# Kernel optimization log

Hardware: AMD Instinct MI355X
Metric: run time of the kernel (lower is better)

Reference implementation:

```python
import jax, jax.numpy as jnp
import numpy as np

B, N, D, H = 8, 1024, 512, 8
HD = D // H
SCALE = 1.0 / np.sqrt(HD).astype(np.float32)


def setup_inputs() -> dict:
    key = jax.random.key(0)
    ks = jax.random.split(key, 7)
    x = jax.random.normal(ks[0], (B, N, D), dtype=jnp.float32)
    U = jax.random.normal(ks[1], (N, N), dtype=jnp.float32)
    attn_mask = jax.random.uniform(ks[2], (B, 1, 1, N), dtype=jnp.float32)
    # learned params: qkv projection D->3D and output projection D->D (with bias)
    w_qkv = jax.random.normal(ks[3], (D, 3 * D), dtype=jnp.float32) / np.sqrt(D).astype(np.float32)
    b_qkv = jnp.zeros((3 * D,), dtype=jnp.float32)
    w_out = jax.random.normal(ks[4], (D, D), dtype=jnp.float32) / np.sqrt(D).astype(np.float32)
    b_out = jnp.zeros((D,), dtype=jnp.float32)
    return {"x": x, "U": U, "attn_mask": attn_mask,
            "w_qkv": w_qkv, "b_qkv": b_qkv, "w_out": w_out, "b_out": b_out}


def reference(x, U, attn_mask, w_qkv, b_qkv, w_out, b_out):
    # QKV projection (QuantIdentity layers are identity in math; key_value = x)
    qkv = x @ w_qkv + b_qkv                       # [B, N, 3D]
    q, k, v = jnp.split(qkv, 3, axis=-1)          # each [B, N, D]

    def split_heads(t):
        return t.reshape(B, N, H, HD).transpose(0, 2, 1, 3)  # [B, H, N, HD]

    qh, kh, vh = split_heads(q), split_heads(k), split_heads(v)
    scores = jnp.einsum('bhqd,bhkd->bhqk', qh, kh) * SCALE   # [B, H, N, N]
    scores = scores + U[None, None, :, :]                    # additive interaction bias
    scores = scores + attn_mask                              # [B,1,1,N] broadcast add
    attn = jax.nn.softmax(scores, axis=-1)
    ctx = jnp.einsum('bhqk,bhkd->bhqd', attn, vh)            # [B, H, N, HD]
    ctx = ctx.transpose(0, 2, 1, 3).reshape(B, N, D)         # merge heads
    out = ctx @ w_out + b_out                                # [B, N, D]
    return out
```

## Files before the change

kernel.cpp:

```cpp
#include <hip/hip_runtime.h>

#define DEV __device__ __forceinline__

typedef __attribute__((ext_vector_type(8))) __bf16 bf16x8;
typedef __attribute__((ext_vector_type(4))) __bf16 bf16x4;
typedef __attribute__((ext_vector_type(4))) float f32x4;
typedef __attribute__((ext_vector_type(4))) float float4v;

typedef __attribute__((address_space(1))) const void ga_void;
typedef __attribute__((address_space(3))) void la_void;

constexpr float LOG2E = 1.44269504089f;
constexpr float ATT_SCALE2 = 0.125f * 1.44269504089f;

#if __has_builtin(__builtin_amdgcn_exp2f)
#define EXP2(x) __builtin_amdgcn_exp2f(x)
#else
#define EXP2(x) exp2f(x)
#endif

DEV void gload16(const void* g, void* l) {
  __builtin_amdgcn_global_load_lds((ga_void*)g, (la_void*)l, 16, 0, 0);
}

DEV f32x4 mfma_bf16(bf16x8 a, bf16x8 b, f32x4 c) {
  return __builtin_amdgcn_mfma_f32_16x16x32_bf16(a, b, c, 0, 0, 0);
}

__global__ __launch_bounds__(256) void cast_x_kernel(
    const float* __restrict__ in, __bf16* __restrict__ out, int n4) {
  int i = blockIdx.x * blockDim.x + threadIdx.x;
  int stride = gridDim.x * blockDim.x;
  for (; i < n4; i += stride) {
    float4v v = ((const float4v*)in)[i];
    bf16x4 o;
    o[0] = (__bf16)v[0]; o[1] = (__bf16)v[1];
    o[2] = (__bf16)v[2]; o[3] = (__bf16)v[3];
    ((bf16x4*)out)[i] = o;
  }
}

__global__ __launch_bounds__(256) void transpose_cast_kernel(
    const float* __restrict__ in, __bf16* __restrict__ out, int K, int Nc) {
  __shared__ float tile[32][33];
  int bx = blockIdx.x * 32;
  int by = blockIdx.y * 32;
  int tx = threadIdx.x, ty = threadIdx.y;
#pragma unroll
  for (int i = ty; i < 32; i += 8)
    tile[i][tx] = in[(size_t)(by + i) * Nc + bx + tx];
  __syncthreads();
#pragma unroll
  for (int i = ty; i < 32; i += 8)
    out[(size_t)(bx + i) * K + by + tx] = (__bf16)tile[tx][i];
}

__global__ __launch_bounds__(256) void gemm_qkv_kernel(
    const __bf16* __restrict__ A, const __bf16* __restrict__ Bt,
    const float* __restrict__ bias,
    __bf16* __restrict__ Qo, __bf16* __restrict__ Ko, __bf16* __restrict__ Vto) {
  __shared__ __align__(16) __bf16 As[2][128 * 32];
  __shared__ __align__(16) __bf16 Bs[2][128 * 32];
  const int tid = threadIdx.x;
  const int lane = tid & 63;
  const int w = tid >> 6;
  const int lr = lane & 15, lg = lane >> 4;
  const int m0 = blockIdx.x * 128, n0 = blockIdx.y * 128;
  const int wr = w >> 1, wc = w & 1;

  f32x4 acc[4][4] = {};

  auto stage = [&](int buf, int kt) {
#pragma unroll
    for (int cc = 0; cc < 2; ++cc) {
      int c = w * 2 + cc;
      int row = c * 16 + (lane >> 2);
      int slot = (lane & 3) ^ ((row >> 1) & 3);
      gload16(A + (size_t)(m0 + row) * 512 + kt * 32 + slot * 8, &As[buf][c * 512]);
      gload16(Bt + (size_t)(n0 + row) * 512 + kt * 32 + slot * 8, &Bs[buf][c * 512]);
    }
  };

  stage(0, 0);
  __syncthreads();
  for (int kt = 0; kt < 16; ++kt) {
    int cur = kt & 1;
    if (kt < 15) stage(cur ^ 1, kt + 1);
    bf16x8 av[4], bv[4];
#pragma unroll
    for (int i = 0; i < 4; ++i) {
      int row = wr * 64 + i * 16 + lr;
      av[i] = *(const bf16x8*)&As[cur][row * 32 + ((lg ^ ((row >> 1) & 3)) * 8)];
    }
#pragma unroll
    for (int j = 0; j < 4; ++j) {
      int row = wc * 64 + j * 16 + lr;
      bv[j] = *(const bf16x8*)&Bs[cur][row * 32 + ((lg ^ ((row >> 1) & 3)) * 8)];
    }
#pragma unroll
    for (int i = 0; i < 4; ++i)
#pragma unroll
      for (int j = 0; j < 4; ++j)
        acc[i][j] = mfma_bf16(av[i], bv[j], acc[i][j]);
    __syncthreads();
  }

  const int sec = n0 >> 9;
#pragma unroll
  for (int j = 0; j < 4; ++j) {
    int n = n0 + wc * 64 + j * 16 + lr;
    float bsv = bias[n];
    int nn = n & 511;
    int h = nn >> 6, d = nn & 63;
#pragma unroll
    for (int i = 0; i < 4; ++i) {
#pragma unroll
      for (int r = 0; r < 4; ++r) {
        int m = m0 + wr * 64 + i * 16 + lg * 4 + r;
        int b = m >> 10, nr = m & 1023;
        float v = acc[i][j][r] + bsv;
        if (sec == 0)
          Qo[(((size_t)(b * 8 + h)) * 1024 + nr) * 64 + d] = (__bf16)v;
        else if (sec == 1)
          Ko[(((size_t)(b * 8 + h)) * 1024 + nr) * 64 + d] = (__bf16)v;
        else
          Vto[(((size_t)(b * 8 + h)) * 64 + d) * 1024 + nr] = (__bf16)v;
      }
    }
  }
}

__global__ __launch_bounds__(256) void gemm_out_kernel(
    const __bf16* __restrict__ A, const __bf16* __restrict__ Bt,
    const float* __restrict__ bias, float* __restrict__ out) {
  __shared__ __align__(16) __bf16 As[2][64 * 32];
  __shared__ __align__(16) __bf16 Bs[2][64 * 32];
  const int tid = threadIdx.x;
  const int lane = tid & 63;
  const int w = tid >> 6;
  const int lr = lane & 15, lg = lane >> 4;
  const int m0 = blockIdx.x * 64, n0 = blockIdx.y * 64;

  f32x4 acc[4] = {};

  auto stage = [&](int buf, int kt) {
    int row = tid >> 2;
    int sg = (tid & 3) ^ ((row >> 1) & 3);
    gload16(A + (size_t)(m0 + row) * 512 + kt * 32 + sg * 8, &As[buf][tid * 8]);
    gload16(Bt + (size_t)(n0 + row) * 512 + kt * 32 + sg * 8, &Bs[buf][tid * 8]);
  };

  stage(0, 0);
  __syncthreads();
  for (int kt = 0; kt < 16; ++kt) {
    int cur = kt & 1;
    if (kt < 15) stage(cur ^ 1, kt + 1);
    int arow = w * 16 + lr;
    bf16x8 av = *(const bf16x8*)&As[cur][arow * 32 + ((lg ^ ((arow >> 1) & 3)) * 8)];
#pragma unroll
    for (int j = 0; j < 4; ++j) {
      int brow = j * 16 + lr;
      bf16x8 bv = *(const bf16x8*)&Bs[cur][brow * 32 + ((lg ^ ((brow >> 1) & 3)) * 8)];
      acc[j] = mfma_bf16(av, bv, acc[j]);
    }
    __syncthreads();
  }

#pragma unroll
  for (int j = 0; j < 4; ++j) {
    int n = n0 + j * 16 + lr;
    float bsv = bias[n];
#pragma unroll
    for (int r = 0; r < 4; ++r) {
      int m = m0 + w * 16 + lg * 4 + r;
      out[(size_t)m * 512 + n] = acc[j][r] + bsv;
    }
  }
}

__global__ __launch_bounds__(256, 4) void attn_kernel(
    const __bf16* __restrict__ Qh, const __bf16* __restrict__ Kh,
    const __bf16* __restrict__ Vth, const float* __restrict__ U,
    const float* __restrict__ mask, __bf16* __restrict__ ctx) {
  __shared__ __align__(16) __bf16 Ks[2][64 * 64];
  __shared__ __align__(16) __bf16 Vs[2][64 * 64];
  __shared__ __align__(16) __bf16 Ps[4][16 * 64];
  const int tid = threadIdx.x;
  const int lane = tid & 63;
  const int w = tid >> 6;
  const int lr = lane & 15, lg = lane >> 4;
  const int bh = blockIdx.x, qb = blockIdx.y;
  const int b = bh >> 3, h = bh & 7;

  const int qrow = qb * 64 + w * 16 + lr;

  bf16x8 qf[2];
  {
    const __bf16* qp = Qh + ((size_t)bh * 1024 + qrow) * 64;
    qf[0] = *(const bf16x8*)(qp + lg * 8);
    qf[1] = *(const bf16x8*)(qp + 32 + lg * 8);
  }

  f32x4 acc_o[4] = {};
  float m_run = -3e38f, l_run = 0.f;

  auto stageKV = [&](int buf, int kb) {
#pragma unroll
    for (int i = 0; i < 2; ++i) {
      int gid = i * 256 + tid;
      int row = gid >> 3, slot = gid & 7;
      int sg = slot ^ (row & 7);
      gload16(Kh + ((size_t)bh * 1024 + kb * 64 + row) * 64 + sg * 8,
              &Ks[buf][(i * 256 + w * 64) * 8]);
      gload16(Vth + ((size_t)bh * 64 + row) * 1024 + kb * 64 + sg * 8,
              &Vs[buf][(i * 256 + w * 64) * 8]);
    }
  };

  const float* Uq = U + (size_t)qrow * 1024 + lg * 4;
  const float* mq = mask + b * 1024 + lg * 4;
  __bf16* pw = &Ps[w][0];

  stageKV(0, 0);
  __builtin_amdgcn_sched_barrier(0);
  asm volatile("s_waitcnt vmcnt(0)" ::: "memory");
  __builtin_amdgcn_s_barrier();
  asm volatile("" ::: "memory");
  __builtin_amdgcn_sched_barrier(0);

  for (int kb = 0; kb < 16; ++kb) {
    const int cur = kb & 1;
    if (kb < 15) stageKV(cur ^ 1, kb + 1);
    __builtin_amdgcn_sched_barrier(0);

    float4v uc[4], mc[4];
#pragma unroll
    for (int t = 0; t < 4; ++t) {
      uc[t] = *(const float4v*)(Uq + kb * 64 + t * 16);
      mc[t] = *(const float4v*)(mq + kb * 64 + t * 16);
    }

    f32x4 sv[4];
    __builtin_amdgcn_s_setprio(1);
#pragma unroll
    for (int t = 0; t < 4; ++t) {
      int krow = t * 16 + lr;
      const __bf16* kp = &Ks[cur][krow * 64];
      int sw = krow & 7;
      bf16x8 k0 = *(const bf16x8*)(kp + ((lg ^ sw) * 8));
      bf16x8 k1 = *(const bf16x8*)(kp + (((4 + lg) ^ sw) * 8));
      f32x4 z = {0.f, 0.f, 0.f, 0.f};
      z = mfma_bf16(k0, qf[0], z);
      z = mfma_bf16(k1, qf[1], z);
      sv[t] = z;
    }
    __builtin_amdgcn_s_setprio(0);

#pragma unroll
    for (int t = 0; t < 4; ++t)
#pragma unroll
      for (int r = 0; r < 4; ++r)
        sv[t][r] = fmaf(uc[t][r], LOG2E, fmaf(sv[t][r], ATT_SCALE2, mc[t][r] * LOG2E));

    float mx = sv[0][0];
#pragma unroll
    for (int t = 0; t < 4; ++t)
#pragma unroll
      for (int r = 0; r < 4; ++r) mx = fmaxf(mx, sv[t][r]);
    mx = fmaxf(mx, __shfl_xor(mx, 16));
    mx = fmaxf(mx, __shfl_xor(mx, 32));

    if (__any(mx > m_run + 8.f)) {
      float mnew = fmaxf(m_run, mx);
      float f = EXP2(m_run - mnew);
      m_run = mnew;
      l_run *= f;
#pragma unroll
      for (int t = 0; t < 4; ++t) acc_o[t] *= f;
    }

    float ps = 0.f;
#pragma unroll
    for (int t = 0; t < 4; ++t)
#pragma unroll
      for (int r = 0; r < 4; ++r) {
        float p = EXP2(sv[t][r] - m_run);
        sv[t][r] = p;
        ps += p;
      }
    ps += __shfl_xor(ps, 16);
    ps += __shfl_xor(ps, 32);
    l_run += ps;

#pragma unroll
    for (int t = 0; t < 4; ++t) {
      bf16x4 pk;
      pk[0] = (__bf16)sv[t][0]; pk[1] = (__bf16)sv[t][1];
      pk[2] = (__bf16)sv[t][2]; pk[3] = (__bf16)sv[t][3];
      int k0 = t * 16 + lg * 4;
      *(bf16x4*)&pw[lr * 64 + (k0 ^ ((lr & 7) << 3))] = pk;
    }

    bf16x8 pa0, pa1;
    {
      const __bf16* pp = &pw[lr * 64];
      int sw = lr & 7;
      pa0 = *(const bf16x8*)(pp + ((lg ^ sw) * 8));
      pa1 = *(const bf16x8*)(pp + (((4 + lg) ^ sw) * 8));
    }
    __builtin_amdgcn_s_setprio(1);
#pragma unroll
    for (int t = 0; t < 4; ++t) {
      int vrow = t * 16 + lr;
      const __bf16* vp = &Vs[cur][vrow * 64];
      int sw = vrow & 7;
      bf16x8 v0 = *(const bf16x8*)(vp + ((lg ^ sw) * 8));
      bf16x8 v1 = *(const bf16x8*)(vp + (((4 + lg) ^ sw) * 8));
      acc_o[t] = mfma_bf16(v0, pa0, acc_o[t]);
      acc_o[t] = mfma_bf16(v1, pa1, acc_o[t]);
    }
    __builtin_amdgcn_s_setprio(0);

    if (kb < 15) {
      __builtin_amdgcn_sched_barrier(0);
      asm volatile("s_waitcnt vmcnt(0)" ::: "memory");
      __builtin_amdgcn_s_barrier();
      asm volatile("" ::: "memory");
      __builtin_amdgcn_sched_barrier(0);
    }
  }

  float inv = 1.0f / l_run;
  __bf16* cp = ctx + ((size_t)(b * 1024 + qrow)) * 512 + h * 64 + lg * 4;
#pragma unroll
  for (int t = 0; t < 4; ++t) {
    bf16x4 ov;
    ov[0] = (__bf16)(acc_o[t][0] * inv); ov[1] = (__bf16)(acc_o[t][1] * inv);
    ov[2] = (__bf16)(acc_o[t][2] * inv); ov[3] = (__bf16)(acc_o[t][3] * inv);
    *(bf16x4*)(cp + t * 16) = ov;
  }
}

extern "C" void kernel_launch(void* const* d_in, const int* in_sizes, int n_in,
                              void* d_out, int out_size, void* d_ws, size_t ws_size,
                              hipStream_t stream) {
  (void)in_sizes; (void)n_in; (void)out_size; (void)ws_size;
  const float* x     = (const float*)d_in[0];
  const float* U     = (const float*)d_in[1];
  const float* mask  = (const float*)d_in[2];
  const float* w_qkv = (const float*)d_in[3];
  const float* b_qkv = (const float*)d_in[4];
  const float* w_out = (const float*)d_in[5];
  const float* b_out = (const float*)d_in[6];
  float* out = (float*)d_out;

  char* p = (char*)d_ws;
  __bf16* xb    = (__bf16*)p; p += (size_t)8192 * 512 * 2;
  __bf16* wqkvT = (__bf16*)p; p += (size_t)1536 * 512 * 2;
  __bf16* woutT = (__bf16*)p; p += (size_t)512 * 512 * 2;
  __bf16* Qh    = (__bf16*)p; p += (size_t)64 * 1024 * 64 * 2;
  __bf16* Kh    = (__bf16*)p; p += (size_t)64 * 1024 * 64 * 2;
  __bf16* Vth   = (__bf16*)p; p += (size_t)64 * 64 * 1024 * 2;
  __bf16* ctx   = (__bf16*)p; p += (size_t)8192 * 512 * 2;

  hipLaunchKernelGGL(cast_x_kernel, dim3(2048), dim3(256), 0, stream,
                     x, xb, 8192 * 512 / 4);
  hipLaunchKernelGGL(transpose_cast_kernel, dim3(48, 16), dim3(32, 8), 0, stream,
                     w_qkv, wqkvT, 512, 1536);
  hipLaunchKernelGGL(transpose_cast_kernel, dim3(16, 16), dim3(32, 8), 0, stream,
                     w_out, woutT, 512, 512);
  hipLaunchKernelGGL(gemm_qkv_kernel, dim3(64, 12), dim3(256), 0, stream,
                     xb, wqkvT, b_qkv, Qh, Kh, Vth);
  hipLaunchKernelGGL(attn_kernel, dim3(64, 16), dim3(256), 0, stream,
                     Qh, Kh, Vth, U, mask, ctx);
  hipLaunchKernelGGL(gemm_out_kernel, dim3(128, 8), dim3(256), 0, stream,
                     ctx, woutT, b_out, out);
}
```

Before: 105.0 us.

## Software-pipeline PV of previous block with QK of current block in attention loop

Splits K and V staging so that the V tile for block kb+1 is loaded after the end-of-iteration barrier. The P·V MFMAs for block kb-1 are deferred and interleaved after the QK MFMAs of block kb, with a tail step after the loop. The U and mask tiles are prefetched one iteration ahead into registers, and the max and sum reductions are rewritten as trees for more parallelism. The aim is to overlap softmax work with matrix-core work and hide global-load latency, at the cost of extra registers and a more complex buffer schedule.

```diff
diff --git a/kernel.cpp b/kernel.cpp
--- a/kernel.cpp
+++ b/kernel.cpp
@@ -204,7 +204,7 @@
   f32x4 acc_o[4] = {};
   float m_run = -3e38f, l_run = 0.f;
 
-  auto stageKV = [&](int buf, int kb) {
+  auto stageK = [&](int buf, int kb) {
 #pragma unroll
     for (int i = 0; i < 2; ++i) {
       int gid = i * 256 + tid;
@@ -212,6 +212,14 @@
       int sg = slot ^ (row & 7);
       gload16(Kh + ((size_t)bh * 1024 + kb * 64 + row) * 64 + sg * 8,
               &Ks[buf][(i * 256 + w * 64) * 8]);
+    }
+  };
+  auto stageV = [&](int buf, int kb) {
+#pragma unroll
+    for (int i = 0; i < 2; ++i) {
+      int gid = i * 256 + tid;
+      int row = gid >> 3, slot = gid & 7;
+      int sg = slot ^ (row & 7);
       gload16(Vth + ((size_t)bh * 64 + row) * 1024 + kb * 64 + sg * 8,
               &Vs[buf][(i * 256 + w * 64) * 8]);
     }
@@ -221,7 +229,14 @@
   const float* mq = mask + b * 1024 + lg * 4;
   __bf16* pw = &Ps[w][0];
 
-  stageKV(0, 0);
+  stageK(0, 0);
+  stageV(0, 0);
+  float4v uc[4], mc[4], ucN[4], mcN[4];
+#pragma unroll
+  for (int t = 0; t < 4; ++t) {
+    uc[t] = *(const float4v*)(Uq + t * 16);
+    mc[t] = *(const float4v*)(mq + t * 16);
+  }
   __builtin_amdgcn_sched_barrier(0);
   asm volatile("s_waitcnt vmcnt(0)" ::: "memory");
   __builtin_amdgcn_s_barrier();
@@ -230,15 +245,15 @@
 
   for (int kb = 0; kb < 16; ++kb) {
     const int cur = kb & 1;
-    if (kb < 15) stageKV(cur ^ 1, kb + 1);
+    if (kb < 15) {
+      stageK(cur ^ 1, kb + 1);
+#pragma unroll
+      for (int t = 0; t < 4; ++t) {
+        ucN[t] = *(const float4v*)(Uq + (kb + 1) * 64 + t * 16);
+        mcN[t] = *(const float4v*)(mq + (kb + 1) * 64 + t * 16);
+      }
+    }
     __builtin_amdgcn_sched_barrier(0);
-
-    float4v uc[4], mc[4];
-#pragma unroll
-    for (int t = 0; t < 4; ++t) {
-      uc[t] = *(const float4v*)(Uq + kb * 64 + t * 16);
-      mc[t] = *(const float4v*)(mq + kb * 64 + t * 16);
-    }
 
     f32x4 sv[4];
     __builtin_amdgcn_s_setprio(1);
@@ -256,17 +271,40 @@
     }
     __builtin_amdgcn_s_setprio(0);
 
+    if (kb > 0) {
+      const int prev = cur ^ 1;
+      bf16x8 pa0, pa1;
+      {
+        const __bf16* pp = &pw[lr * 64];
+        int sw = lr & 7;
+        pa0 = *(const bf16x8*)(pp + ((lg ^ sw) * 8));
+        pa1 = *(const bf16x8*)(pp + (((4 + lg) ^ sw) * 8));
+      }
+      __builtin_amdgcn_s_setprio(1);
+#pragma unroll
+      for (int t = 0; t < 4; ++t) {
+        int vrow = t * 16 + lr;
+        const __bf16* vp = &Vs[prev][vrow * 64];
+        int sw = vrow & 7;
+        bf16x8 v0 = *(const bf16x8*)(vp + ((lg ^ sw) * 8));
+        bf16x8 v1 = *(const bf16x8*)(vp + (((4 + lg) ^ sw) * 8));
+        acc_o[t] = mfma_bf16(v0, pa0, acc_o[t]);
+        acc_o[t] = mfma_bf16(v1, pa1, acc_o[t]);
+      }
+      __builtin_amdgcn_s_setprio(0);
+    }
+
 #pragma unroll
     for (int t = 0; t < 4; ++t)
 #pragma unroll
       for (int r = 0; r < 4; ++r)
         sv[t][r] = fmaf(uc[t][r], LOG2E, fmaf(sv[t][r], ATT_SCALE2, mc[t][r] * LOG2E));
 
-    float mx = sv[0][0];
+    float mt[4];
 #pragma unroll
     for (int t = 0; t < 4; ++t)
-#pragma unroll
-      for (int r = 0; r < 4; ++r) mx = fmaxf(mx, sv[t][r]);
+      mt[t] = fmaxf(fmaxf(sv[t][0], sv[t][1]), fmaxf(sv[t][2], sv[t][3]));
+    float mx = fmaxf(fmaxf(mt[0], mt[1]), fmaxf(mt[2], mt[3]));
     mx = fmaxf(mx, __shfl_xor(mx, 16));
     mx = fmaxf(mx, __shfl_xor(mx, 32));
 
@@ -279,15 +317,14 @@
       for (int t = 0; t < 4; ++t) acc_o[t] *= f;
     }
 
-    float ps = 0.f;
-#pragma unroll
-    for (int t = 0; t < 4; ++t)
-#pragma unroll
-      for (int r = 0; r < 4; ++r) {
-        float p = EXP2(sv[t][r] - m_run);
-        sv[t][r] = p;
-        ps += p;
-      }
+    float pt[4];
+#pragma unroll
+    for (int t = 0; t < 4; ++t) {
+#pragma unroll
+      for (int r = 0; r < 4; ++r) sv[t][r] = EXP2(sv[t][r] - m_run);
+      pt[t] = (sv[t][0] + sv[t][1]) + (sv[t][2] + sv[t][3]);
+    }
+    float ps = (pt[0] + pt[1]) + (pt[2] + pt[3]);
     ps += __shfl_xor(ps, 16);
     ps += __shfl_xor(ps, 32);
     l_run += ps;
@@ -301,6 +338,21 @@
       *(bf16x4*)&pw[lr * 64 + (k0 ^ ((lr & 7) << 3))] = pk;
     }
 
+    if (kb < 15) {
+#pragma unroll
+      for (int t = 0; t < 4; ++t) { uc[t] = ucN[t]; mc[t] = mcN[t]; }
+    }
+
+    __builtin_amdgcn_sched_barrier(0);
+    asm volatile("s_waitcnt vmcnt(0)" ::: "memory");
+    __builtin_amdgcn_s_barrier();
+    asm volatile("" ::: "memory");
+    __builtin_amdgcn_sched_barrier(0);
+
+    if (kb < 15) stageV(cur ^ 1, kb + 1);
+  }
+
+  {
     bf16x8 pa0, pa1;
     {
       const __bf16* pp = &pw[lr * 64];
@@ -308,25 +360,15 @@
       pa0 = *(const bf16x8*)(pp + ((lg ^ sw) * 8));
       pa1 = *(const bf16x8*)(pp + (((4 + lg) ^ sw) * 8));
     }
-    __builtin_amdgcn_s_setprio(1);
 #pragma unroll
     for (int t = 0; t < 4; ++t) {
       int vrow = t * 16 + lr;
-      const __bf16* vp = &Vs[cur][vrow * 64];
+      const __bf16* vp = &Vs[1][vrow * 64];
       int sw = vrow & 7;
       bf16x8 v0 = *(const bf16x8*)(vp + ((lg ^ sw) * 8));
       bf16x8 v1 = *(const bf16x8*)(vp + (((4 + lg) ^ sw) * 8));
       acc_o[t] = mfma_bf16(v0, pa0, acc_o[t]);
       acc_o[t] = mfma_bf16(v1, pa1, acc_o[t]);
-    }
-    __builtin_amdgcn_s_setprio(0);
-
-    if (kb < 15) {
-      __builtin_amdgcn_sched_barrier(0);
-      asm volatile("s_waitcnt vmcnt(0)" ::: "memory");
-      __builtin_amdgcn_s_barrier();
-      asm volatile("" ::: "memory");
-      __builtin_amdgcn_sched_barrier(0);
     }
   }
 
```

New measurement: 105.4 us. Within noise of the previous version (+0.3%).

## Process two query tiles per attention block to reuse staged K/V

Applied to the files above, without the earlier changes.

Each attention workgroup now handles two 64-row query tiles (qp and qp+8) and shares every staged K/V tile between them, halving the grid and the total K/V global-to-LDS traffic and barrier count per query. The P buffer is doubled per wave and launch bounds drop to 2 blocks per CU to make room for the larger register state. The trade is higher register pressure, lower occupancy and only 512 workgroups, which may leave CUs underfilled or cause spills.

```diff
diff --git a/kernel.cpp b/kernel.cpp
--- a/kernel.cpp
+++ b/kernel.cpp
@@ -178,31 +178,34 @@
   }
 }
 
-__global__ __launch_bounds__(256, 4) void attn_kernel(
+__global__ __launch_bounds__(256, 2) void attn_kernel(
     const __bf16* __restrict__ Qh, const __bf16* __restrict__ Kh,
     const __bf16* __restrict__ Vth, const float* __restrict__ U,
     const float* __restrict__ mask, __bf16* __restrict__ ctx) {
   __shared__ __align__(16) __bf16 Ks[2][64 * 64];
   __shared__ __align__(16) __bf16 Vs[2][64 * 64];
-  __shared__ __align__(16) __bf16 Ps[4][16 * 64];
+  __shared__ __align__(16) __bf16 Ps[4][2][16 * 64];
   const int tid = threadIdx.x;
   const int lane = tid & 63;
   const int w = tid >> 6;
   const int lr = lane & 15, lg = lane >> 4;
-  const int bh = blockIdx.x, qb = blockIdx.y;
+  const int bh = blockIdx.x, qp = blockIdx.y;
   const int b = bh >> 3, h = bh & 7;
 
-  const int qrow = qb * 64 + w * 16 + lr;
-
-  bf16x8 qf[2];
-  {
-    const __bf16* qp = Qh + ((size_t)bh * 1024 + qrow) * 64;
-    qf[0] = *(const bf16x8*)(qp + lg * 8);
-    qf[1] = *(const bf16x8*)(qp + 32 + lg * 8);
-  }
-
-  f32x4 acc_o[4] = {};
-  float m_run = -3e38f, l_run = 0.f;
+  int qrow[2];
+  qrow[0] = qp * 64 + w * 16 + lr;
+  qrow[1] = (qp + 8) * 64 + w * 16 + lr;
+
+  bf16x8 qf[2][2];
+#pragma unroll
+  for (int it = 0; it < 2; ++it) {
+    const __bf16* qpt = Qh + ((size_t)bh * 1024 + qrow[it]) * 64;
+    qf[it][0] = *(const bf16x8*)(qpt + lg * 8);
+    qf[it][1] = *(const bf16x8*)(qpt + 32 + lg * 8);
+  }
+
+  f32x4 acc_o[2][4] = {};
+  float m_run[2] = {-3e38f, -3e38f}, l_run[2] = {0.f, 0.f};
 
   auto stageKV = [&](int buf, int kb) {
 #pragma unroll
@@ -217,9 +220,9 @@
     }
   };
 
-  const float* Uq = U + (size_t)qrow * 1024 + lg * 4;
+  const float* Uq0 = U + (size_t)qrow[0] * 1024 + lg * 4;
+  const float* Uq1 = U + (size_t)qrow[1] * 1024 + lg * 4;
   const float* mq = mask + b * 1024 + lg * 4;
-  __bf16* pw = &Ps[w][0];
 
   stageKV(0, 0);
   __builtin_amdgcn_sched_barrier(0);
@@ -231,16 +234,16 @@
   for (int kb = 0; kb < 16; ++kb) {
     const int cur = kb & 1;
     if (kb < 15) stageKV(cur ^ 1, kb + 1);
-    __builtin_amdgcn_sched_barrier(0);
-
-    float4v uc[4], mc[4];
+
+    float4v uc[2][4], mc[4];
 #pragma unroll
     for (int t = 0; t < 4; ++t) {
-      uc[t] = *(const float4v*)(Uq + kb * 64 + t * 16);
       mc[t] = *(const float4v*)(mq + kb * 64 + t * 16);
-    }
-
-    f32x4 sv[4];
+      uc[0][t] = *(const float4v*)(Uq0 + kb * 64 + t * 16);
+      uc[1][t] = *(const float4v*)(Uq1 + kb * 64 + t * 16);
+    }
+
+    f32x4 sv[2][4];
     __builtin_amdgcn_s_setprio(1);
 #pragma unroll
     for (int t = 0; t < 4; ++t) {
@@ -249,64 +252,72 @@
       int sw = krow & 7;
       bf16x8 k0 = *(const bf16x8*)(kp + ((lg ^ sw) * 8));
       bf16x8 k1 = *(const bf16x8*)(kp + (((4 + lg) ^ sw) * 8));
-      f32x4 z = {0.f, 0.f, 0.f, 0.f};
-      z = mfma_bf16(k0, qf[0], z);
-      z = mfma_bf16(k1, qf[1], z);
-      sv[t] = z;
+#pragma unroll
+      for (int it = 0; it < 2; ++it) {
+        f32x4 z = {0.f, 0.f, 0.f, 0.f};
+        z = mfma_bf16(k0, qf[it][0], z);
+        z = mfma_bf16(k1, qf[it][1], z);
+        sv[it][t] = z;
+      }
     }
     __builtin_amdgcn_s_setprio(0);
 
 #pragma unroll
-    for (int t = 0; t < 4; ++t)
-#pragma unroll
-      for (int r = 0; r < 4; ++r)
-        sv[t][r] = fmaf(uc[t][r], LOG2E, fmaf(sv[t][r], ATT_SCALE2, mc[t][r] * LOG2E));
-
-    float mx = sv[0][0];
-#pragma unroll
-    for (int t = 0; t < 4; ++t)
-#pragma unroll
-      for (int r = 0; r < 4; ++r) mx = fmaxf(mx, sv[t][r]);
-    mx = fmaxf(mx, __shfl_xor(mx, 16));
-    mx = fmaxf(mx, __shfl_xor(mx, 32));
-
-    if (__any(mx > m_run + 8.f)) {
-      float mnew = fmaxf(m_run, mx);
-      float f = EXP2(m_run - mnew);
-      m_run = mnew;
-      l_run *= f;
-#pragma unroll
-      for (int t = 0; t < 4; ++t) acc_o[t] *= f;
-    }
-
-    float ps = 0.f;
-#pragma unroll
-    for (int t = 0; t < 4; ++t)
-#pragma unroll
-      for (int r = 0; r < 4; ++r) {
-        float p = EXP2(sv[t][r] - m_run);
-        sv[t][r] = p;
-        ps += p;
-      }
-    ps += __shfl_xor(ps, 16);
-    ps += __shfl_xor(ps, 32);
-    l_run += ps;
-
-#pragma unroll
-    for (int t = 0; t < 4; ++t) {
-      bf16x4 pk;
-      pk[0] = (__bf16)sv[t][0]; pk[1] = (__bf16)sv[t][1];
-      pk[2] = (__bf16)sv[t][2]; pk[3] = (__bf16)sv[t][3];
-      int k0 = t * 16 + lg * 4;
-      *(bf16x4*)&pw[lr * 64 + (k0 ^ ((lr & 7) << 3))] = pk;
-    }
-
-    bf16x8 pa0, pa1;
-    {
-      const __bf16* pp = &pw[lr * 64];
+    for (int it = 0; it < 2; ++it) {
+#pragma unroll
+      for (int t = 0; t < 4; ++t)
+#pragma unroll
+        for (int r = 0; r < 4; ++r)
+          sv[it][t][r] =
+              fmaf(uc[it][t][r], LOG2E, fmaf(sv[it][t][r], ATT_SCALE2, mc[t][r] * LOG2E));
+
+      float mt[4];
+#pragma unroll
+      for (int t = 0; t < 4; ++t)
+        mt[t] = fmaxf(fmaxf(sv[it][t][0], sv[it][t][1]), fmaxf(sv[it][t][2], sv[it][t][3]));
+      float mx = fmaxf(fmaxf(mt[0], mt[1]), fmaxf(mt[2], mt[3]));
+      mx = fmaxf(mx, __shfl_xor(mx, 16));
+      mx = fmaxf(mx, __shfl_xor(mx, 32));
+
+      if (__any(mx > m_run[it] + 8.f)) {
+        float mnew = fmaxf(m_run[it], mx);
+        float f = EXP2(m_run[it] - mnew);
+        m_run[it] = mnew;
+        l_run[it] *= f;
+#pragma unroll
+        for (int t = 0; t < 4; ++t) acc_o[it][t] *= f;
+      }
+
+      float pt[4];
+#pragma unroll
+      for (int t = 0; t < 4; ++t) {
+#pragma unroll
+        for (int r = 0; r < 4; ++r) sv[it][t][r] = EXP2(sv[it][t][r] - m_run[it]);
+        pt[t] = (sv[it][t][0] + sv[it][t][1]) + (sv[it][t][2] + sv[it][t][3]);
+      }
+      float ps = (pt[0] + pt[1]) + (pt[2] + pt[3]);
+      ps += __shfl_xor(ps, 16);
+      ps += __shfl_xor(ps, 32);
+      l_run[it] += ps;
+
+      __bf16* pw = &Ps[w][it][0];
+#pragma unroll
+      for (int t = 0; t < 4; ++t) {
+        bf16x4 pk;
+        pk[0] = (__bf16)sv[it][t][0]; pk[1] = (__bf16)sv[it][t][1];
+        pk[2] = (__bf16)sv[it][t][2]; pk[3] = (__bf16)sv[it][t][3];
+        int k0 = t * 16 + lg * 4;
+        *(bf16x4*)&pw[lr * 64 + (k0 ^ ((lr & 7) << 3))] = pk;
+      }
+    }
+
+    bf16x8 pa[2][2];
+#pragma unroll
+    for (int it = 0; it < 2; ++it) {
+      const __bf16* pp = &Ps[w][it][lr * 64];
       int sw = lr & 7;
-      pa0 = *(const bf16x8*)(pp + ((lg ^ sw) * 8));
-      pa1 = *(const bf16x8*)(pp + (((4 + lg) ^ sw) * 8));
+      pa[it][0] = *(const bf16x8*)(pp + ((lg ^ sw) * 8));
+      pa[it][1] = *(const bf16x8*)(pp + (((4 + lg) ^ sw) * 8));
     }
     __builtin_amdgcn_s_setprio(1);
 #pragma unroll
@@ -316,28 +327,32 @@
       int sw = vrow & 7;
       bf16x8 v0 = *(const bf16x8*)(vp + ((lg ^ sw) * 8));
       bf16x8 v1 = *(const bf16x8*)(vp + (((4 + lg) ^ sw) * 8));
-      acc_o[t] = mfma_bf16(v0, pa0, acc_o[t]);
-      acc_o[t] = mfma_bf16(v1, pa1, acc_o[t]);
+#pragma unroll
+      for (int it = 0; it < 2; ++it) {
+        acc_o[it][t] = mfma_bf16(v0, pa[it][0], acc_o[it][t]);
+        acc_o[it][t] = mfma_bf16(v1, pa[it][1], acc_o[it][t]);
+      }
     }
     __builtin_amdgcn_s_setprio(0);
 
-    if (kb < 15) {
-      __builtin_amdgcn_sched_barrier(0);
-      asm volatile("s_waitcnt vmcnt(0)" ::: "memory");
-      __builtin_amdgcn_s_barrier();
-      asm volatile("" ::: "memory");
-      __builtin_amdgcn_sched_barrier(0);
-    }
-  }
-
-  float inv = 1.0f / l_run;
-  __bf16* cp = ctx + ((size_t)(b * 1024 + qrow)) * 512 + h * 64 + lg * 4;
-#pragma unroll
-  for (int t = 0; t < 4; ++t) {
-    bf16x4 ov;
-    ov[0] = (__bf16)(acc_o[t][0] * inv); ov[1] = (__bf16)(acc_o[t][1] * inv);
-    ov[2] = (__bf16)(acc_o[t][2] * inv); ov[3] = (__bf16)(acc_o[t][3] * inv);
-    *(bf16x4*)(cp + t * 16) = ov;
+    __builtin_amdgcn_sched_barrier(0);
+    asm volatile("s_waitcnt vmcnt(0)" ::: "memory");
+    __builtin_amdgcn_s_barrier();
+    asm volatile("" ::: "memory");
+    __builtin_amdgcn_sched_barrier(0);
+  }
+
+#pragma unroll
+  for (int it = 0; it < 2; ++it) {
+    float inv = 1.0f / l_run[it];
+    __bf16* cp = ctx + ((size_t)(b * 1024 + qrow[it])) * 512 + h * 64 + lg * 4;
+#pragma unroll
+    for (int t = 0; t < 4; ++t) {
+      bf16x4 ov;
+      ov[0] = (__bf16)(acc_o[it][t][0] * inv); ov[1] = (__bf16)(acc_o[it][t][1] * inv);
+      ov[2] = (__bf16)(acc_o[it][t][2] * inv); ov[3] = (__bf16)(acc_o[it][t][3] * inv);
+      *(bf16x4*)(cp + t * 16) = ov;
+    }
   }
 }
 
@@ -371,7 +386,7 @@
                      w_out, woutT, 512, 512);
   hipLaunchKernelGGL(gemm_qkv_kernel, dim3(64, 12), dim3(256), 0, stream,
                      xb, wqkvT, b_qkv, Qh, Kh, Vth);
-  hipLaunchKernelGGL(attn_kernel, dim3(64, 16), dim3(256), 0, stream,
+  hipLaunchKernelGGL(attn_kernel, dim3(64, 8), dim3(256), 0, stream,
                      Qh, Kh, Vth, U, mask, ctx);
   hipLaunchKernelGGL(gemm_out_kernel, dim3(128, 8), dim3(256), 0, stream,
                      ctx, woutT, b_out, out);
```

Measured after the change: 99.01 us. 1.06x faster.

## Load K/V fragments directly from global memory and merge weight transposes

Applied to the files above, without the earlier changes.

The attention kernel drops its double-buffered LDS staging of K and V tiles along with the per-iteration barriers. Each wave now reads its K and V MFMA fragments straight from global memory and relies on L1/L2 for reuse across the four waves. The two weight transpose launches are merged into one kernel, and the max and sum reductions become tree-shaped. The risk is more global traffic and load latency that is no longer hidden by prefetch, in exchange for fewer barriers and less LDS use, which may allow higher occupancy.

```diff
diff --git a/kernel.cpp b/kernel.cpp
--- a/kernel.cpp
+++ b/kernel.cpp
@@ -40,10 +40,15 @@
   }
 }
 
-__global__ __launch_bounds__(256) void transpose_cast_kernel(
-    const float* __restrict__ in, __bf16* __restrict__ out, int K, int Nc) {
+__global__ __launch_bounds__(256) void transpose_both_kernel(
+    const float* __restrict__ wqkv, const float* __restrict__ wout,
+    __bf16* __restrict__ wqkvT, __bf16* __restrict__ woutT) {
   __shared__ float tile[32][33];
-  int bx = blockIdx.x * 32;
+  const float* in;
+  __bf16* out;
+  int Nc, bx;
+  if (blockIdx.x < 48) { in = wqkv; out = wqkvT; Nc = 1536; bx = blockIdx.x * 32; }
+  else                 { in = wout; out = woutT; Nc = 512;  bx = (blockIdx.x - 48) * 32; }
   int by = blockIdx.y * 32;
   int tx = threadIdx.x, ty = threadIdx.y;
 #pragma unroll
@@ -52,7 +57,7 @@
   __syncthreads();
 #pragma unroll
   for (int i = ty; i < 32; i += 8)
-    out[(size_t)(bx + i) * K + by + tx] = (__bf16)tile[tx][i];
+    out[(size_t)(bx + i) * 512 + by + tx] = (__bf16)tile[tx][i];
 }
 
 __global__ __launch_bounds__(256) void gemm_qkv_kernel(
@@ -182,8 +187,6 @@
     const __bf16* __restrict__ Qh, const __bf16* __restrict__ Kh,
     const __bf16* __restrict__ Vth, const float* __restrict__ U,
     const float* __restrict__ mask, __bf16* __restrict__ ctx) {
-  __shared__ __align__(16) __bf16 Ks[2][64 * 64];
-  __shared__ __align__(16) __bf16 Vs[2][64 * 64];
   __shared__ __align__(16) __bf16 Ps[4][16 * 64];
   const int tid = threadIdx.x;
   const int lane = tid & 63;
@@ -204,35 +207,13 @@
   f32x4 acc_o[4] = {};
   float m_run = -3e38f, l_run = 0.f;
 
-  auto stageKV = [&](int buf, int kb) {
-#pragma unroll
-    for (int i = 0; i < 2; ++i) {
-      int gid = i * 256 + tid;
-      int row = gid >> 3, slot = gid & 7;
-      int sg = slot ^ (row & 7);
-      gload16(Kh + ((size_t)bh * 1024 + kb * 64 + row) * 64 + sg * 8,
-              &Ks[buf][(i * 256 + w * 64) * 8]);
-      gload16(Vth + ((size_t)bh * 64 + row) * 1024 + kb * 64 + sg * 8,
-              &Vs[buf][(i * 256 + w * 64) * 8]);
-    }
-  };
-
+  const __bf16* Kbase = Kh + (size_t)bh * 1024 * 64;
+  const __bf16* Vbase = Vth + (size_t)bh * 64 * 1024;
   const float* Uq = U + (size_t)qrow * 1024 + lg * 4;
   const float* mq = mask + b * 1024 + lg * 4;
   __bf16* pw = &Ps[w][0];
 
-  stageKV(0, 0);
-  __builtin_amdgcn_sched_barrier(0);
-  asm volatile("s_waitcnt vmcnt(0)" ::: "memory");
-  __builtin_amdgcn_s_barrier();
-  asm volatile("" ::: "memory");
-  __builtin_amdgcn_sched_barrier(0);
-
   for (int kb = 0; kb < 16; ++kb) {
-    const int cur = kb & 1;
-    if (kb < 15) stageKV(cur ^ 1, kb + 1);
-    __builtin_amdgcn_sched_barrier(0);
-
     float4v uc[4], mc[4];
 #pragma unroll
     for (int t = 0; t < 4; ++t) {
@@ -245,10 +226,9 @@
 #pragma unroll
     for (int t = 0; t < 4; ++t) {
       int krow = t * 16 + lr;
-      const __bf16* kp = &Ks[cur][krow * 64];
-      int sw = krow & 7;
-      bf16x8 k0 = *(const bf16x8*)(kp + ((lg ^ sw) * 8));
-      bf16x8 k1 = *(const bf16x8*)(kp + (((4 + lg) ^ sw) * 8));
+      const __bf16* kp = Kbase + (size_t)(kb * 64 + krow) * 64;
+      bf16x8 k0 = *(const bf16x8*)(kp + lg * 8);
+      bf16x8 k1 = *(const bf16x8*)(kp + 32 + lg * 8);
       f32x4 z = {0.f, 0.f, 0.f, 0.f};
       z = mfma_bf16(k0, qf[0], z);
       z = mfma_bf16(k1, qf[1], z);
@@ -262,11 +242,11 @@
       for (int r = 0; r < 4; ++r)
         sv[t][r] = fmaf(uc[t][r], LOG2E, fmaf(sv[t][r], ATT_SCALE2, mc[t][r] * LOG2E));
 
-    float mx = sv[0][0];
+    float mt[4];
 #pragma unroll
     for (int t = 0; t < 4; ++t)
-#pragma unroll
-      for (int r = 0; r < 4; ++r) mx = fmaxf(mx, sv[t][r]);
+      mt[t] = fmaxf(fmaxf(sv[t][0], sv[t][1]), fmaxf(sv[t][2], sv[t][3]));
+    float mx = fmaxf(fmaxf(mt[0], mt[1]), fmaxf(mt[2], mt[3]));
     mx = fmaxf(mx, __shfl_xor(mx, 16));
     mx = fmaxf(mx, __shfl_xor(mx, 32));
 
@@ -279,15 +259,14 @@
       for (int t = 0; t < 4; ++t) acc_o[t] *= f;
     }
 
-    float ps = 0.f;
-#pragma unroll
-    for (int t = 0; t < 4; ++t)
-#pragma unroll
-      for (int r = 0; r < 4; ++r) {
-        float p = EXP2(sv[t][r] - m_run);
-        sv[t][r] = p;
-        ps += p;
-      }
+    float pt[4];
+#pragma unroll
+    for (int t = 0; t < 4; ++t) {
+#pragma unroll
+      for (int r = 0; r < 4; ++r) sv[t][r] = EXP2(sv[t][r] - m_run);
+      pt[t] = (sv[t][0] + sv[t][1]) + (sv[t][2] + sv[t][3]);
+    }
+    float ps = (pt[0] + pt[1]) + (pt[2] + pt[3]);
     ps += __shfl_xor(ps, 16);
     ps += __shfl_xor(ps, 32);
     l_run += ps;
@@ -312,22 +291,13 @@
 #pragma unroll
     for (int t = 0; t < 4; ++t) {
       int vrow = t * 16 + lr;
-      const __bf16* vp = &Vs[cur][vrow * 64];
-      int sw = vrow & 7;
-      bf16x8 v0 = *(const bf16x8*)(vp + ((lg ^ sw) * 8));
-      bf16x8 v1 = *(const bf16x8*)(vp + (((4 + lg) ^ sw) * 8));
+      const __bf16* vp = Vbase + (size_t)vrow * 1024 + kb * 64;
+      bf16x8 v0 = *(const bf16x8*)(vp + lg * 8);
+      bf16x8 v1 = *(const bf16x8*)(vp + 32 + lg * 8);
       acc_o[t] = mfma_bf16(v0, pa0, acc_o[t]);
       acc_o[t] = mfma_bf16(v1, pa1, acc_o[t]);
     }
     __builtin_amdgcn_s_setprio(0);
-
-    if (kb < 15) {
-      __builtin_amdgcn_sched_barrier(0);
-      asm volatile("s_waitcnt vmcnt(0)" ::: "memory");
-      __builtin_amdgcn_s_barrier();
-      asm volatile("" ::: "memory");
-      __builtin_amdgcn_sched_barrier(0);
-    }
   }
 
   float inv = 1.0f / l_run;
@@ -365,10 +335,8 @@
 
   hipLaunchKernelGGL(cast_x_kernel, dim3(2048), dim3(256), 0, stream,
                      x, xb, 8192 * 512 / 4);
-  hipLaunchKernelGGL(transpose_cast_kernel, dim3(48, 16), dim3(32, 8), 0, stream,
-                     w_qkv, wqkvT, 512, 1536);
-  hipLaunchKernelGGL(transpose_cast_kernel, dim3(16, 16), dim3(32, 8), 0, stream,
-                     w_out, woutT, 512, 512);
+  hipLaunchKernelGGL(transpose_both_kernel, dim3(64, 16), dim3(32, 8), 0, stream,
+                     w_qkv, w_out, wqkvT, woutT);
   hipLaunchKernelGGL(gemm_qkv_kernel, dim3(64, 12), dim3(256), 0, stream,
                      xb, wqkvT, b_qkv, Qh, Kh, Vth);
   hipLaunchKernelGGL(attn_kernel, dim3(64, 16), dim3(256), 0, stream,
```

Result: slower. 199.6 us (+90.0%).
